# Kernel tuning notes

Hardware: AMD Instinct MI355X
Metric: run time of the kernel (lower is better)

The kernel has to match this reference:

```python
import jax, jax.numpy as jnp
import numpy as np

N_NODES = 50000
N_PATHS = 4
N_EDGES = 800000
D_IN = 256
D_OUT = 256
D_HID = 128  # SemanticAttention default hidden_size


def setup_inputs() -> dict:
    key = jax.random.key(0)
    ks = jax.random.split(key, 6)
    x = jax.random.normal(ks[0], (N_NODES, D_IN), dtype=jnp.float32)
    edge_indices = jax.random.randint(ks[1], (N_PATHS, 2, N_EDGES), 0, N_NODES)
    Ws = jax.random.normal(ks[2], (N_PATHS, D_IN, D_OUT), dtype=jnp.float32) * (1.0 / np.sqrt(D_IN))
    bs = jnp.zeros((N_PATHS, D_OUT), dtype=jnp.float32)
    attn_w1 = jax.random.normal(ks[3], (D_OUT, D_HID), dtype=jnp.float32) * (1.0 / np.sqrt(D_OUT))
    attn_b1 = jnp.zeros((D_HID,), dtype=jnp.float32)
    attn_w2 = jax.random.normal(ks[4], (D_HID, 1), dtype=jnp.float32) * (1.0 / np.sqrt(D_HID))
    return {"x": x, "edge_indices": edge_indices, "Ws": Ws, "bs": bs,
            "attn_w1": attn_w1, "attn_b1": attn_b1, "attn_w2": attn_w2}


def _gcn_conv(x, W, b, edges):
    """PyG GCNConv with normalize=True, add_self_loops=True.
    out = D^{-1/2} (A + I) D^{-1/2} (x @ W) + b
    """
    n = x.shape[0]
    xw = x @ W  # [N, D_OUT]
    loop = jnp.arange(n, dtype=edges.dtype)
    src = jnp.concatenate([edges[0], loop])
    dst = jnp.concatenate([edges[1], loop])
    ones = jnp.ones(src.shape[0], dtype=x.dtype)
    deg = jax.ops.segment_sum(ones, dst, num_segments=n)  # in-degree incl. self loop
    dinv = jnp.where(deg > 0, jax.lax.rsqrt(deg), 0.0)
    norm = dinv[src] * dinv[dst]  # [E+N]
    msgs = xw[src] * norm[:, None]  # gather + scale
    return jax.ops.segment_sum(msgs, dst, num_segments=n) + b  # scatter-add


def reference(x, edge_indices, Ws, bs, attn_w1, attn_b1, attn_w2):
    P = edge_indices.shape[0]
    # per-meta-path GCN embeddings, stacked -> [N, P, D_OUT]
    z = jnp.stack([_gcn_conv(x, Ws[i], bs[i], edge_indices[i]) for i in range(P)], axis=1)
    # semantic attention: per-node softmax over meta-paths
    w = jnp.tanh(z @ attn_w1 + attn_b1) @ attn_w2  # [N, P, 1]
    beta = jax.nn.softmax(w, axis=1)
    return (beta * z).sum(axis=1)  # [N, D_OUT]
```

## Files before the change

### kernel.cpp

```cpp
#include <hip/hip_runtime.h>
#include <hip/hip_fp16.h>
#include <cstdint>
#include <cstddef>

#define NN 50000
#define NE 800000
#define NP 4
#define DD 256
#define HH 128
#define MPAD 50048

#define NB 196
#define CAP 5120
#define EPB 4096
#define NBB ((NE + EPB - 1) / EPB)
#define BIN_BLOCKS (NBB * NP)

typedef _Float16 f16x8 __attribute__((ext_vector_type(8)));
typedef float f32x4 __attribute__((ext_vector_type(4)));

#define X_OCT (NN * DD / 8)
#define W_OCT (NP * DD * DD / 8)
#define W1_OCT (HH * DD / 8)
#define CVT_BLOCKS ((X_OCT + W_OCT + W1_OCT + 255) / 256)
#define GEMM_BLOCKS ((MPAD / 64) * NP)

__global__ __launch_bounds__(256) void k_bin(const int* __restrict__ edges,
                                             int* __restrict__ gcnt,
                                             unsigned int* __restrict__ binned,
                                             const float* __restrict__ x,
                                             const float* __restrict__ Ws,
                                             const float* __restrict__ w1,
                                             _Float16* __restrict__ xh,
                                             _Float16* __restrict__ Wt,
                                             _Float16* __restrict__ w1t) {
    const int bx = blockIdx.x;
    const int tid = threadIdx.x;
    if (bx < BIN_BLOCKS) {
        __shared__ int hist[256], lb[256], cur[256], gbase[256], wsum[4];
        __shared__ unsigned int stage[EPB];
        const int p  = bx / NBB;
        const int bc = bx - p * NBB;
        const int e0 = bc * EPB;
        const int total = min(EPB, NE - e0);
        const int* es = edges + (size_t)p * 2 * NE;
        const int* ed = es + NE;
        hist[tid] = 0;
        __syncthreads();
        unsigned int word[16];
        int bkt[16];
#pragma unroll
        for (int j = 0; j < 16; j++) {
            int e = e0 + j * 256 + tid;
            bkt[j] = -1;
            if (e < NE) {
                int dst = ed[e];
                int src = es[e];
                int b = dst >> 8;
                bkt[j] = b;
                word[j] = ((unsigned)b << 24) | ((unsigned)(dst & 255) << 16) | (unsigned)src;
                atomicAdd(&hist[b], 1);
            }
        }
        __syncthreads();
        const int lane = tid & 63, wv = tid >> 6;
        int v = hist[tid];
        int incl = v;
#pragma unroll
        for (int off = 1; off < 64; off <<= 1) {
            int u = __shfl_up(incl, off);
            if (lane >= off) incl += u;
        }
        if (lane == 63) wsum[wv] = incl;
        __syncthreads();
        int wbase = 0;
        for (int i = 0; i < wv; i++) wbase += wsum[i];
        int excl = wbase + incl - v;
        lb[tid] = excl;
        cur[tid] = excl;
        if (tid < NB && v > 0) gbase[tid] = atomicAdd(&gcnt[p * NB + tid], v);
        __syncthreads();
#pragma unroll
        for (int j = 0; j < 16; j++)
            if (bkt[j] >= 0) {
                int r = atomicAdd(&cur[bkt[j]], 1);
                stage[r] = word[j];
            }
        __syncthreads();
        for (int s = tid; s < total; s += 256) {
            unsigned int wd = stage[s];
            int b = wd >> 24;
            int posl = gbase[b] + (s - lb[b]);
            if (posl < CAP)
                binned[(size_t)(p * NB + b) * CAP + posl] = wd & 0x00FFFFFFu;
        }
        return;
    }
    int i = (bx - BIN_BLOCKS) * 256 + tid;
    if (i < X_OCT) {
        const float4* src = (const float4*)x + (size_t)i * 2;
        float4 v0 = src[0], v1 = src[1];
        f16x8 o;
        o[0] = (_Float16)v0.x; o[1] = (_Float16)v0.y; o[2] = (_Float16)v0.z; o[3] = (_Float16)v0.w;
        o[4] = (_Float16)v1.x; o[5] = (_Float16)v1.y; o[6] = (_Float16)v1.z; o[7] = (_Float16)v1.w;
        *((f16x8*)xh + i) = o;
    } else if (i < X_OCT + W_OCT) {
        int j = i - X_OCT;
        int p   = j / (DD * DD / 8);
        int rem = j - p * (DD * DD / 8);
        int n   = rem >> 5;
        int k8  = (rem & 31) * 8;
        const float* wp = Ws + (size_t)p * DD * DD;
        f16x8 o;
#pragma unroll
        for (int t = 0; t < 8; t++) o[t] = (_Float16)wp[(size_t)(k8 + t) * DD + n];
        *((f16x8*)(Wt + (size_t)p * DD * DD + (size_t)n * DD + k8)) = o;
    } else if (i < X_OCT + W_OCT + W1_OCT) {
        int j = i - X_OCT - W_OCT;
        int n  = j >> 5;
        int k8 = (j & 31) * 8;
        f16x8 o;
#pragma unroll
        for (int t = 0; t < 8; t++) o[t] = (_Float16)w1[(size_t)(k8 + t) * HH + n];
        *((f16x8*)(w1t + (size_t)n * DD + k8)) = o;
    }
}

__global__ __launch_bounds__(256) void k_sort(const int* __restrict__ gcnt,
                                              const unsigned int* __restrict__ binned,
                                              unsigned short* __restrict__ srcs,
                                              int* __restrict__ offs,
                                              int* __restrict__ ends,
                                              float* __restrict__ dinv) {
    __shared__ int hist[256], cur[256], wsum[4];
    __shared__ unsigned short sorted[CAP];
    const int bx = blockIdx.x;
    const int tid = threadIdx.x;
    const int p = bx / NB, b = bx - p * NB;
    const size_t base = (size_t)bx * CAP;
    const int n = min(gcnt[bx], CAP);
    hist[tid] = 0;
    __syncthreads();
    unsigned int w[20];
#pragma unroll
    for (int j = 0; j < 20; j++) {
        int s = j * 256 + tid;
        w[j] = 0xFFFFFFFFu;
        if (s < n) {
            w[j] = binned[base + s];
            atomicAdd(&hist[(w[j] >> 16) & 255], 1);
        }
    }
    __syncthreads();
    const int lane = tid & 63, wv = tid >> 6;
    int v = hist[tid];
    int incl = v;
#pragma unroll
    for (int off = 1; off < 64; off <<= 1) {
        int u = __shfl_up(incl, off);
        if (lane >= off) incl += u;
    }
    if (lane == 63) wsum[wv] = incl;
    __syncthreads();
    int wbase = 0;
    for (int i = 0; i < wv; i++) wbase += wsum[i];
    int excl = wbase + incl - v;
    cur[tid] = excl;
    const int node = b * 256 + tid;
    if (node < NN) {
        int o = (int)base + excl;
        offs[p * NN + node] = o;
        ends[p * NN + node] = o + v;
        dinv[p * NN + node] = rsqrtf((float)v + 1.0f);
    }
    __syncthreads();
#pragma unroll
    for (int j = 0; j < 20; j++)
        if (w[j] != 0xFFFFFFFFu) {
            int r = atomicAdd(&cur[(w[j] >> 16) & 255], 1);
            sorted[r] = (unsigned short)(w[j] & 0xFFFFu);
        }
    __syncthreads();
#pragma unroll
    for (int j = 0; j < 20; j++) {
        int s = j * 256 + tid;
        if (s < n) srcs[base + s] = sorted[s];
    }
}

__global__ __launch_bounds__(256) void k_gemm(const _Float16* __restrict__ xh,
                                              const _Float16* __restrict__ Wt,
                                              const float* __restrict__ dinv,
                                              _Float16* __restrict__ xws) {
    const int gb   = blockIdx.x;
    const int p    = gb / (MPAD / 64);
    const int bm   = gb - p * (MPAD / 64);
    const int wv   = threadIdx.x >> 6;
    const int lane = threadIdx.x & 63;
    const int m_base = bm * 64;
    const int n0   = wv * 64;
    const int mr   = lane & 15;
    const int quad = lane >> 4;

    const _Float16* ap = xh + (size_t)(m_base + mr) * DD + quad * 8;
    const _Float16* bp = Wt + (size_t)p * DD * DD + (size_t)(n0 + mr) * DD + quad * 8;
    const float* dv = dinv + (size_t)p * NN;
    _Float16* cp = xws + (size_t)p * NN * DD;

    f32x4 acc[4][4] = {};
    for (int k0 = 0; k0 < DD; k0 += 32) {
        f16x8 a[4], b[4];
#pragma unroll
        for (int i = 0; i < 4; i++) a[i] = *(const f16x8*)(ap + (size_t)i * 16 * DD + k0);
#pragma unroll
        for (int j = 0; j < 4; j++) b[j] = *(const f16x8*)(bp + (size_t)j * 16 * DD + k0);
#pragma unroll
        for (int i = 0; i < 4; i++)
#pragma unroll
            for (int j = 0; j < 4; j++)
                acc[i][j] = __builtin_amdgcn_mfma_f32_16x16x32_f16(a[i], b[j], acc[i][j], 0, 0, 0);
    }
#pragma unroll
    for (int i = 0; i < 4; i++) {
#pragma unroll
        for (int r = 0; r < 4; r++) {
            int row = m_base + i * 16 + quad * 4 + r;
            if (row < NN) {
                float d = dv[row];
#pragma unroll
                for (int j = 0; j < 4; j++)
                    cp[(size_t)row * DD + n0 + j * 16 + mr] = (_Float16)(d * acc[i][j][r]);
            }
        }
    }
}

__global__ __launch_bounds__(512) void k_fused(const _Float16* __restrict__ xws,
                                               const float* __restrict__ dinv,
                                               const int* __restrict__ offs,
                                               const int* __restrict__ ends,
                                               const unsigned short* __restrict__ srcs,
                                               const float* __restrict__ bs,
                                               const _Float16* __restrict__ w1t,
                                               const float* __restrict__ b1,
                                               const float* __restrict__ w2,
                                               float* __restrict__ out) {
    const int w    = threadIdx.x >> 6;
    const int lane = threadIdx.x & 63;
    const int quad = lane >> 4, mr = lane & 15;
    const int half = lane >> 5, hl = lane & 31;

    __shared__ __align__(16) _Float16 zs[64][264];

    union U { f16x8 v; int i4[4]; };

#pragma unroll 1
    for (int q = 0; q < 2; q++) {
        const int n = blockIdx.x * 16 + w * 2 + q;
#pragma unroll 1
        for (int p = 0; p < NP; p++) {
            const _Float16* xp = xws + (size_t)p * NN * DD;
            U acc;
#pragma unroll
            for (int t = 0; t < 4; t++) acc.i4[t] = 0;
            if (half == 0)
                acc.v = *(const f16x8*)(xp + (size_t)n * DD + hl * 8);
            int k  = offs[p * NN + n];
            int ke = ends[p * NN + n];
            for (; k + 8 <= ke; k += 8) {
                int s0 = srcs[k + half];
                int s1 = srcs[k + 2 + half];
                int s2 = srcs[k + 4 + half];
                int s3 = srcs[k + 6 + half];
                f16x8 v0 = *(const f16x8*)(xp + (size_t)s0 * DD + hl * 8);
                f16x8 v1 = *(const f16x8*)(xp + (size_t)s1 * DD + hl * 8);
                f16x8 v2 = *(const f16x8*)(xp + (size_t)s2 * DD + hl * 8);
                f16x8 v3 = *(const f16x8*)(xp + (size_t)s3 * DD + hl * 8);
                acc.v += (v0 + v1) + (v2 + v3);
            }
            for (; k + 2 <= ke; k += 2) {
                int s0 = srcs[k + half];
                acc.v += *(const f16x8*)(xp + (size_t)s0 * DD + hl * 8);
            }
            if (k < ke && half == 0)
                acc.v += *(const f16x8*)(xp + (size_t)srcs[k] * DD + hl * 8);
            U other;
#pragma unroll
            for (int t = 0; t < 4; t++) other.i4[t] = __shfl_xor(acc.i4[t], 32);
            acc.v += other.v;
            if (half == 0) {
                float dvv = dinv[p * NN + n];
                int row = (w * 2 + q) * 4 + p;
                f16x8 zo;
#pragma unroll
                for (int t = 0; t < 8; t++)
                    zo[t] = (_Float16)(dvv * (float)acc.v[t] + bs[p * DD + hl * 8 + t]);
                *(f16x8*)&zs[row][hl * 8] = zo;
            }
        }
    }

    __syncthreads();
    if (w >= 4) return;

    f32x4 acch[8] = {};
    for (int k0 = 0; k0 < DD; k0 += 32) {
        f16x8 a = *(const f16x8*)&zs[w * 16 + mr][k0 + quad * 8];
#pragma unroll
        for (int j = 0; j < 8; j++) {
            f16x8 b = *(const f16x8*)(w1t + (size_t)(j * 16 + mr) * DD + k0 + quad * 8);
            acch[j] = __builtin_amdgcn_mfma_f32_16x16x32_f16(a, b, acch[j], 0, 0, 0);
        }
    }

    float part[4] = {};
#pragma unroll
    for (int j = 0; j < 8; j++) {
        int col = j * 16 + mr;
        float bb = b1[col], ww = w2[col];
#pragma unroll
        for (int r = 0; r < 4; r++)
            part[r] += tanhf(acch[j][r] + bb) * ww;
    }
#pragma unroll
    for (int off = 1; off < 16; off <<= 1) {
#pragma unroll
        for (int r = 0; r < 4; r++) part[r] += __shfl_xor(part[r], off);
    }
    float m = fmaxf(fmaxf(part[0], part[1]), fmaxf(part[2], part[3]));
    float e0 = __expf(part[0] - m), e1 = __expf(part[1] - m),
          e2 = __expf(part[2] - m), e3 = __expf(part[3] - m);
    float rr = 1.0f / (e0 + e1 + e2 + e3);
    float be[4] = {e0 * rr, e1 * rr, e2 * rr, e3 * rr};

    const int n  = blockIdx.x * 16 + w * 4 + quad;
    const int rb = w * 16 + quad * 4;
    float o[16] = {};
#pragma unroll
    for (int p = 0; p < 4; p++) {
        f16x8 z0 = *(const f16x8*)&zs[rb + p][mr * 16];
        f16x8 z1 = *(const f16x8*)&zs[rb + p][mr * 16 + 8];
#pragma unroll
        for (int t = 0; t < 8; t++) {
            o[t]     += be[p] * (float)z0[t];
            o[t + 8] += be[p] * (float)z1[t];
        }
    }
#pragma unroll
    for (int t = 0; t < 16; t += 4)
        *(float4*)(out + (size_t)n * DD + mr * 16 + t) =
            make_float4(o[t], o[t + 1], o[t + 2], o[t + 3]);
}

extern "C" void kernel_launch(void* const* d_in, const int* in_sizes, int n_in,
                              void* d_out, int out_size, void* d_ws, size_t ws_size,
                              hipStream_t stream) {
    const float* x     = (const float*)d_in[0];
    const int*   edges = (const int*)d_in[1];
    const float* Ws    = (const float*)d_in[2];
    const float* bs    = (const float*)d_in[3];
    const float* w1    = (const float*)d_in[4];
    const float* b1    = (const float*)d_in[5];
    const float* w2    = (const float*)d_in[6];
    float* out = (float*)d_out;

    char* ws = (char*)d_ws;
    int*            gcnt   = (int*)ws;
    unsigned int*   binned = (unsigned int*)(ws + (1 << 20));
    unsigned short* srcs   = (unsigned short*)(ws + (18 << 20));
    float*          dinv   = (float*)(ws + (27 << 20));
    int*            offs   = (int*)(ws + (28 << 20));
    int*            ends   = (int*)(ws + (29 << 20));
    _Float16*       Wt     = (_Float16*)(ws + (30 << 20));
    _Float16*       w1t    = (_Float16*)(ws + (30 << 20) + (1 << 19));
    _Float16*       xh     = (_Float16*)(ws + (31 << 20));
    _Float16*       xws    = (_Float16*)(ws + (57 << 20));

    hipMemsetAsync(gcnt, 0, NP * NB * sizeof(int), stream);

    k_bin<<<BIN_BLOCKS + CVT_BLOCKS, 256, 0, stream>>>(
        edges, gcnt, binned, x, Ws, w1, xh, Wt, w1t);

    k_sort<<<NP * NB, 256, 0, stream>>>(gcnt, binned, srcs, offs, ends, dinv);

    k_gemm<<<GEMM_BLOCKS, 256, 0, stream>>>(xh, Wt, dinv, xws);

    k_fused<<<NN / 16, 512, 0, stream>>>(xws, dinv, offs, ends, srcs,
                                         bs, w1t, b1, w2, out);
}
```

Measured before the change: 552.9 us.

## Pad per-node neighbor lists to multiples of 8 with a zero dummy row

Each node's CSR segment is rounded up to a multiple of 8 and filled with a padding index that points at a zero row appended to the projected features. The gather loop can then run 16-wide unrolled iterations with a single 8-wide tail and no scalar remainder handling. This is meant to cut loop overhead and divergence and to expose more memory-level parallelism in the gather. In exchange it adds wasted gathers of the zero row, a larger srcs buffer, extra shared-memory initialization in the sort, and a changed workspace layout.

```diff
diff --git a/kernel.cpp b/kernel.cpp
--- a/kernel.cpp
+++ b/kernel.cpp
@@ -9,9 +9,11 @@
 #define DD 256
 #define HH 128
 #define MPAD 50048
+#define PADIDX 50000
 
 #define NB 196
 #define CAP 5120
+#define SCAP 6144
 #define EPB 4096
 #define NBB ((NE + EPB - 1) / EPB)
 #define BIN_BLOCKS (NBB * NP)
@@ -20,9 +22,10 @@
 typedef float f32x4 __attribute__((ext_vector_type(4)));
 
 #define X_OCT (NN * DD / 8)
+#define XP_OCT (MPAD * DD / 8)
 #define W_OCT (NP * DD * DD / 8)
 #define W1_OCT (HH * DD / 8)
-#define CVT_BLOCKS ((X_OCT + W_OCT + W1_OCT + 255) / 256)
+#define CVT_BLOCKS ((XP_OCT + W_OCT + W1_OCT + 255) / 256)
 #define GEMM_BLOCKS ((MPAD / 64) * NP)
 
 __global__ __launch_bounds__(256) void k_bin(const int* __restrict__ edges,
@@ -97,15 +100,20 @@
         return;
     }
     int i = (bx - BIN_BLOCKS) * 256 + tid;
-    if (i < X_OCT) {
-        const float4* src = (const float4*)x + (size_t)i * 2;
-        float4 v0 = src[0], v1 = src[1];
+    if (i < XP_OCT) {
         f16x8 o;
-        o[0] = (_Float16)v0.x; o[1] = (_Float16)v0.y; o[2] = (_Float16)v0.z; o[3] = (_Float16)v0.w;
-        o[4] = (_Float16)v1.x; o[5] = (_Float16)v1.y; o[6] = (_Float16)v1.z; o[7] = (_Float16)v1.w;
+        if (i < X_OCT) {
+            const float4* src = (const float4*)x + (size_t)i * 2;
+            float4 v0 = src[0], v1 = src[1];
+            o[0] = (_Float16)v0.x; o[1] = (_Float16)v0.y; o[2] = (_Float16)v0.z; o[3] = (_Float16)v0.w;
+            o[4] = (_Float16)v1.x; o[5] = (_Float16)v1.y; o[6] = (_Float16)v1.z; o[7] = (_Float16)v1.w;
+        } else {
+#pragma unroll
+            for (int t = 0; t < 8; t++) o[t] = (_Float16)0.0f;
+        }
         *((f16x8*)xh + i) = o;
-    } else if (i < X_OCT + W_OCT) {
-        int j = i - X_OCT;
+    } else if (i < XP_OCT + W_OCT) {
+        int j = i - XP_OCT;
         int p   = j / (DD * DD / 8);
         int rem = j - p * (DD * DD / 8);
         int n   = rem >> 5;
@@ -115,8 +123,8 @@
 #pragma unroll
         for (int t = 0; t < 8; t++) o[t] = (_Float16)wp[(size_t)(k8 + t) * DD + n];
         *((f16x8*)(Wt + (size_t)p * DD * DD + (size_t)n * DD + k8)) = o;
-    } else if (i < X_OCT + W_OCT + W1_OCT) {
-        int j = i - X_OCT - W_OCT;
+    } else if (i < XP_OCT + W_OCT + W1_OCT) {
+        int j = i - XP_OCT - W_OCT;
         int n  = j >> 5;
         int k8 = (j & 31) * 8;
         f16x8 o;
@@ -133,13 +141,15 @@
                                               int* __restrict__ ends,
                                               float* __restrict__ dinv) {
     __shared__ int hist[256], cur[256], wsum[4];
-    __shared__ unsigned short sorted[CAP];
+    __shared__ unsigned short sorted[SCAP];
     const int bx = blockIdx.x;
     const int tid = threadIdx.x;
     const int p = bx / NB, b = bx - p * NB;
-    const size_t base = (size_t)bx * CAP;
+    const int base = bx * SCAP;
     const int n = min(gcnt[bx], CAP);
     hist[tid] = 0;
+#pragma unroll
+    for (int j = 0; j < SCAP / 256; j++) sorted[j * 256 + tid] = (unsigned short)PADIDX;
     __syncthreads();
     unsigned int w[20];
 #pragma unroll
@@ -147,14 +157,15 @@
         int s = j * 256 + tid;
         w[j] = 0xFFFFFFFFu;
         if (s < n) {
-            w[j] = binned[base + s];
+            w[j] = binned[(size_t)bx * CAP + s];
             atomicAdd(&hist[(w[j] >> 16) & 255], 1);
         }
     }
     __syncthreads();
     const int lane = tid & 63, wv = tid >> 6;
-    int v = hist[tid];
-    int incl = v;
+    int v  = hist[tid];
+    int pv = (v + 7) & ~7;
+    int incl = pv;
 #pragma unroll
     for (int off = 1; off < 64; off <<= 1) {
         int u = __shfl_up(incl, off);
@@ -164,27 +175,28 @@
     __syncthreads();
     int wbase = 0;
     for (int i = 0; i < wv; i++) wbase += wsum[i];
-    int excl = wbase + incl - v;
+    int excl = wbase + incl - pv;
     cur[tid] = excl;
     const int node = b * 256 + tid;
     if (node < NN) {
-        int o = (int)base + excl;
+        int o = base + excl;
         offs[p * NN + node] = o;
-        ends[p * NN + node] = o + v;
+        ends[p * NN + node] = o + pv;
         dinv[p * NN + node] = rsqrtf((float)v + 1.0f);
     }
     __syncthreads();
+    int totalpad = wsum[0] + wsum[1] + wsum[2] + wsum[3];
 #pragma unroll
     for (int j = 0; j < 20; j++)
         if (w[j] != 0xFFFFFFFFu) {
             int r = atomicAdd(&cur[(w[j] >> 16) & 255], 1);
-            sorted[r] = (unsigned short)(w[j] & 0xFFFFu);
-        }
-    __syncthreads();
-#pragma unroll
-    for (int j = 0; j < 20; j++) {
+            if (r < SCAP) sorted[r] = (unsigned short)(w[j] & 0xFFFFu);
+        }
+    __syncthreads();
+#pragma unroll
+    for (int j = 0; j < SCAP / 256; j++) {
         int s = j * 256 + tid;
-        if (s < n) srcs[base + s] = sorted[s];
+        if (s < totalpad && s < SCAP) srcs[base + s] = sorted[s];
     }
 }
 
@@ -205,7 +217,7 @@
     const _Float16* ap = xh + (size_t)(m_base + mr) * DD + quad * 8;
     const _Float16* bp = Wt + (size_t)p * DD * DD + (size_t)(n0 + mr) * DD + quad * 8;
     const float* dv = dinv + (size_t)p * NN;
-    _Float16* cp = xws + (size_t)p * NN * DD;
+    _Float16* cp = xws + (size_t)p * MPAD * DD;
 
     f32x4 acc[4][4] = {};
     for (int k0 = 0; k0 < DD; k0 += 32) {
@@ -225,12 +237,10 @@
 #pragma unroll
         for (int r = 0; r < 4; r++) {
             int row = m_base + i * 16 + quad * 4 + r;
-            if (row < NN) {
-                float d = dv[row];
-#pragma unroll
-                for (int j = 0; j < 4; j++)
-                    cp[(size_t)row * DD + n0 + j * 16 + mr] = (_Float16)(d * acc[i][j][r]);
-            }
+            float d = (row < NN) ? dv[row] : 0.0f;
+#pragma unroll
+            for (int j = 0; j < 4; j++)
+                cp[(size_t)row * DD + n0 + j * 16 + mr] = (_Float16)(d * acc[i][j][r]);
         }
     }
 }
@@ -259,7 +269,7 @@
         const int n = blockIdx.x * 16 + w * 2 + q;
 #pragma unroll 1
         for (int p = 0; p < NP; p++) {
-            const _Float16* xp = xws + (size_t)p * NN * DD;
+            const _Float16* xp = xws + (size_t)p * MPAD * DD;
             U acc;
 #pragma unroll
             for (int t = 0; t < 4; t++) acc.i4[t] = 0;
@@ -267,23 +277,26 @@
                 acc.v = *(const f16x8*)(xp + (size_t)n * DD + hl * 8);
             int k  = offs[p * NN + n];
             int ke = ends[p * NN + n];
-            for (; k + 8 <= ke; k += 8) {
-                int s0 = srcs[k + half];
-                int s1 = srcs[k + 2 + half];
-                int s2 = srcs[k + 4 + half];
-                int s3 = srcs[k + 6 + half];
-                f16x8 v0 = *(const f16x8*)(xp + (size_t)s0 * DD + hl * 8);
-                f16x8 v1 = *(const f16x8*)(xp + (size_t)s1 * DD + hl * 8);
-                f16x8 v2 = *(const f16x8*)(xp + (size_t)s2 * DD + hl * 8);
-                f16x8 v3 = *(const f16x8*)(xp + (size_t)s3 * DD + hl * 8);
-                acc.v += (v0 + v1) + (v2 + v3);
+            for (; k + 16 <= ke; k += 16) {
+                int s[8];
+#pragma unroll
+                for (int j = 0; j < 8; j++) s[j] = srcs[k + 2 * j + half];
+                f16x8 v[8];
+#pragma unroll
+                for (int j = 0; j < 8; j++)
+                    v[j] = *(const f16x8*)(xp + (size_t)s[j] * DD + hl * 8);
+                acc.v += ((v[0] + v[1]) + (v[2] + v[3])) + ((v[4] + v[5]) + (v[6] + v[7]));
             }
-            for (; k + 2 <= ke; k += 2) {
-                int s0 = srcs[k + half];
-                acc.v += *(const f16x8*)(xp + (size_t)s0 * DD + hl * 8);
+            if (k < ke) {
+                int s[4];
+#pragma unroll
+                for (int j = 0; j < 4; j++) s[j] = srcs[k + 2 * j + half];
+                f16x8 v[4];
+#pragma unroll
+                for (int j = 0; j < 4; j++)
+                    v[j] = *(const f16x8*)(xp + (size_t)s[j] * DD + hl * 8);
+                acc.v += (v[0] + v[1]) + (v[2] + v[3]);
             }
-            if (k < ke && half == 0)
-                acc.v += *(const f16x8*)(xp + (size_t)srcs[k] * DD + hl * 8);
             U other;
 #pragma unroll
             for (int t = 0; t < 4; t++) other.i4[t] = __shfl_xor(acc.i4[t], 32);
@@ -368,13 +381,13 @@
     int*            gcnt   = (int*)ws;
     unsigned int*   binned = (unsigned int*)(ws + (1 << 20));
     unsigned short* srcs   = (unsigned short*)(ws + (18 << 20));
-    float*          dinv   = (float*)(ws + (27 << 20));
-    int*            offs   = (int*)(ws + (28 << 20));
-    int*            ends   = (int*)(ws + (29 << 20));
-    _Float16*       Wt     = (_Float16*)(ws + (30 << 20));
-    _Float16*       w1t    = (_Float16*)(ws + (30 << 20) + (1 << 19));
-    _Float16*       xh     = (_Float16*)(ws + (31 << 20));
-    _Float16*       xws    = (_Float16*)(ws + (57 << 20));
+    float*          dinv   = (float*)(ws + (28 << 20));
+    int*            offs   = (int*)(ws + (29 << 20));
+    int*            ends   = (int*)(ws + (30 << 20));
+    _Float16*       Wt     = (_Float16*)(ws + (31 << 20));
+    _Float16*       w1t    = (_Float16*)(ws + (31 << 20) + (1 << 19));
+    _Float16*       xh     = (_Float16*)(ws + (32 << 20));
+    _Float16*       xws    = (_Float16*)(ws + (58 << 20));
 
     hipMemsetAsync(gcnt, 0, NP * NB * sizeof(int), stream);
 
```

New measurement: 539.6 us. 1.02x faster.
